# Performance work log

Hardware: AMD Instinct MI355X
Metric: run time of the kernel (lower is better)

## Reference

```python
import jax, jax.numpy as jnp
import numpy as np

NA, NB, D, H = 8192, 2048, 192, 4
DK = D // H


def setup_inputs() -> dict:
    key = jax.random.key(0)
    ks = jax.random.split(key, 12)
    a_z = jax.random.normal(ks[0], (NA, D), dtype=jnp.float32)
    bv_z = jax.random.normal(ks[1], (NB, D), dtype=jnp.float32)
    weight = jax.random.normal(ks[2], (NA, NB), dtype=jnp.float32)
    mask = jax.random.randint(ks[3], (NA, NB), 0, 2).astype(bool)
    mask = mask.at[:, 0].set(True)  # every actor has >=1 valid bill (valid_idx == all)
    s = 1.0 / np.sqrt(D)
    Wq = jax.random.normal(ks[4], (D, D), dtype=jnp.float32) * s
    Wk = jax.random.normal(ks[5], (D, D), dtype=jnp.float32) * s
    Wv = jax.random.normal(ks[6], (D, D), dtype=jnp.float32) * s
    Wo = jax.random.normal(ks[7], (D, D), dtype=jnp.float32) * s
    bq = jnp.zeros((D,), jnp.float32)
    bk = jnp.zeros((D,), jnp.float32)
    bvb = jnp.zeros((D,), jnp.float32)
    bo = jnp.zeros((D,), jnp.float32)
    return {"a_z": a_z, "bv_z": bv_z, "weight": weight, "mask": mask,
            "Wq": Wq, "Wk": Wk, "Wv": Wv, "Wo": Wo,
            "bq": bq, "bk": bk, "bvb": bvb, "bo": bo}


def reference(a_z, bv_z, weight, mask, Wq, Wk, Wv, Wo, bq, bk, bvb, bo):
    # ActorHead.forward: per-actor single-query attention over bill versions,
    # with float attn_mask from `weight` and key_padding_mask from `mask`.
    a_z = jnp.nan_to_num(a_z, nan=0.0, posinf=1.0, neginf=-1.0)
    bv_z = jnp.nan_to_num(bv_z, nan=0.0, posinf=1.0, neginf=-1.0)
    w = jnp.nan_to_num(weight, nan=0.0, posinf=1.0, neginf=-1.0)

    q = (a_z @ Wq.T + bq).reshape(NA, H, DK)   # [NA,H,DK]
    k = (bv_z @ Wk.T + bk).reshape(NB, H, DK)  # [NB,H,DK]
    v = (bv_z @ Wv.T + bvb).reshape(NB, H, DK)

    scores = jnp.einsum('ahd,bhd->ahb', q, k) / np.sqrt(DK)  # [NA,H,NB]
    w_masked = jnp.where(mask, w, -jnp.inf)                  # attn_mask (weight.masked_fill)
    kpm = jnp.where(mask, 0.0, -jnp.inf)                     # key_padding_mask as additive bias
    scores = scores + (w_masked + kpm)[:, None, :]

    p = jax.nn.softmax(scores, axis=-1)                      # [NA,H,NB]
    out = jnp.einsum('ahb,bhd->ahd', p, v).reshape(NA, D)
    out = out @ Wo.T + bo
    out = jnp.nan_to_num(out, nan=0.0, posinf=0.0, neginf=0.0)
    topic_align = out.reshape(NA, H, DK).mean(axis=1)        # [NA,DK]

    attn_avg = jnp.nan_to_num(p.mean(axis=1), nan=0.0, posinf=0.0, neginf=0.0)
    attn_avg = attn_avg * mask
    norm_scores = jax.nn.softmax(w_masked, axis=-1)
    norm_scores = jnp.nan_to_num(norm_scores, nan=0.0, posinf=0.0, neginf=0.0) * mask
    influence = jnp.nan_to_num((norm_scores * attn_avg).sum(axis=-1),
                               nan=0.0, posinf=1.0, neginf=-1.0)  # [NA]

    # pack (topic_align, influence) into one array: [NA, DK+1]
    return jnp.concatenate([topic_align, influence[:, None]], axis=-1)
```

## Files before the change

### kernel.cpp

```cpp
#include <hip/hip_runtime.h>
#include <hip/hip_bf16.h>

#define NA 8192
#define NB 2048
#define DIM 192
#define NH 4
#define DKH 48
#define TA 16
#define TB 32
#define PREC 200
#define SCALE 0.14433756729740643f
#define INVSCALE 6.928203230275509f
#define NEGBIG 1e30f

typedef __bf16 bf16x8 __attribute__((ext_vector_type(8)));
typedef float f32x4 __attribute__((ext_vector_type(4)));

#define MFMA16(a, b, c) __builtin_amdgcn_mfma_f32_16x16x32_bf16(a, b, c, 0, 0, 0)

#define GLDS(gp, lp)                                                      \
  __builtin_amdgcn_global_load_lds(                                       \
      (__attribute__((address_space(1))) void*)(const void*)(gp),         \
      (__attribute__((address_space(3))) void*)(void*)(lp), 16, 0, 0)

__device__ __forceinline__ float rsumg(float v) {
  v += __shfl_xor(v, 16, 64);
  v += __shfl_xor(v, 32, 64);
  return v;
}

__global__ __launch_bounds__(256) void prep_kernel(
    const float* __restrict__ a_z, const float* __restrict__ bv_z,
    const float* __restrict__ Wq, const float* __restrict__ Wk, const float* __restrict__ Wv,
    const float* __restrict__ bq, const float* __restrict__ bk, const float* __restrict__ bvb,
    const float* __restrict__ Wo, const float* __restrict__ bo,
    const float* __restrict__ weight, const void* __restrict__ maskp,
    __bf16* __restrict__ Qo, __bf16* __restrict__ Ko, __bf16* __restrict__ Vo,
    float* __restrict__ WoeT, float* __restrict__ boe, int* __restrict__ mflag,
    float* __restrict__ MwG, float* __restrict__ LwG)
{
  const int blk = blockIdx.x;
  const int t = threadIdx.x;

  if (blk < 1536) {
    __shared__ float xs[8][DIM];
    const float* src; const float* W; const float* bias; int row0; int which;
    if (blk < 1024)      { src = a_z;  W = Wq; bias = bq;  row0 = blk * 8;          which = 0; }
    else if (blk < 1280) { src = bv_z; W = Wk; bias = bk;  row0 = (blk - 1024) * 8; which = 1; }
    else                 { src = bv_z; W = Wv; bias = bvb; row0 = (blk - 1280) * 8; which = 2; }
    for (int i = t; i < 8 * 48; i += 256) {
      int r = i / 48, c = i % 48;
      ((float4*)xs[r])[c] = ((const float4*)(src + (size_t)(row0 + r) * DIM))[c];
    }
    __syncthreads();
    if (t < 192) {
      float acc[8];
      float bb = bias[t];
      #pragma unroll
      for (int r = 0; r < 8; ++r) acc[r] = bb;
      const float4* wr = (const float4*)(W + (size_t)t * DIM);
      for (int c = 0; c < 48; ++c) {
        float4 w = wr[c];
        #pragma unroll
        for (int r = 0; r < 8; ++r) {
          float4 x = ((const float4*)xs[r])[c];
          acc[r] += w.x * x.x + w.y * x.y + w.z * x.z + w.w * x.w;
        }
      }
      int h = t / 48, dd = t % 48;
      if (which == 0) {
        #pragma unroll
        for (int r = 0; r < 8; ++r)
          Qo[((size_t)(row0 + r) * 4 + h) * 64 + dd] = (__bf16)acc[r];
      } else if (which == 1) {
        #pragma unroll
        for (int r = 0; r < 8; ++r)
          Ko[((size_t)h * NB + row0 + r) * 64 + dd] = (__bf16)acc[r];
      } else {
        bf16x8 pk;
        #pragma unroll
        for (int r = 0; r < 8; ++r) pk[r] = (__bf16)acc[r];
        *(bf16x8*)(Vo + (size_t)t * NB + row0) = pk;
      }
    }
    if (which == 0) {
      for (int i = t; i < 512; i += 256) {
        int r = i >> 6, hh = (i >> 4) & 3, kk = i & 15;
        Qo[((size_t)(row0 + r) * 4 + hh) * 64 + 48 + kk] = (__bf16)0.f;
      }
    } else if (which == 1) {
      for (int i = t; i < 512; i += 256) {
        int r = i >> 6, hh = (i >> 4) & 3, kk = i & 15;
        Ko[((size_t)hh * NB + row0 + r) * 64 + 48 + kk] = (__bf16)0.f;
      }
    }
  } else if (blk == 1536) {
    __shared__ int fl;
    if (t == 0) fl = 0;
    __syncthreads();
    const unsigned int* mw = (const unsigned int*)maskp;
    for (int i = t; i < 1024; i += 256) {
      unsigned int v = mw[i];
      if (v == 0x3F800000u) atomicMax(&fl, 2);
      else if (v > 1u) atomicMax(&fl, 1);
    }
    __syncthreads();
    if (t == 0) *mflag = fl;
  } else if (blk < 1573) {
    int i = (blk - 1537) * 256 + t;
    if (i < DIM * DKH) {
      int k = i / DKH, d = i % DKH;
      float s = 0.25f * (Wo[(size_t)d * DIM + k] + Wo[(size_t)(d + 48) * DIM + k] +
                         Wo[(size_t)(d + 96) * DIM + k] + Wo[(size_t)(d + 144) * DIM + k]);
      WoeT[k * DKH + d] = s;
    }
    if (i < DKH) boe[i] = 0.25f * (bo[i] + bo[i + 48] + bo[i + 96] + bo[i + 144]);
  } else {
    __shared__ int fl;
    if (t == 0) fl = 0;
    __syncthreads();
    {
      const unsigned int* mw = (const unsigned int*)maskp;
      for (int i = t; i < 1024; i += 256) {
        unsigned int v = mw[i];
        if (v == 0x3F800000u) atomicMax(&fl, 2);
        else if (v > 1u) atomicMax(&fl, 1);
      }
    }
    __syncthreads();
    const int mmode = fl;
    const int lane = t & 63;
    const int a = (blk - 1573) * 4 + (t >> 6);
    const float* wr = weight + (size_t)a * NB;
    const unsigned char* m8 = (const unsigned char*)maskp + (size_t)a * NB;
    const float* mf = (const float*)maskp + (size_t)a * NB;
    const int* m32 = (const int*)maskp + (size_t)a * NB;

    float mloc = -NEGBIG, sloc = 0.f;
    for (int it = 0; it < 8; ++it) {
      int idx = it * 256 + lane * 4;
      float4 w4 = *(const float4*)(wr + idx);
      bool ok0, ok1, ok2, ok3;
      if (mmode == 1) {
        unsigned mm = *(const unsigned*)(m8 + idx);
        ok0 = mm & 0xffu; ok1 = (mm >> 8) & 0xffu; ok2 = (mm >> 16) & 0xffu; ok3 = mm >> 24;
      } else if (mmode == 2) {
        float4 mv = *(const float4*)(mf + idx);
        ok0 = mv.x != 0.f; ok1 = mv.y != 0.f; ok2 = mv.z != 0.f; ok3 = mv.w != 0.f;
      } else {
        int4 mv = *(const int4*)(m32 + idx);
        ok0 = mv.x; ok1 = mv.y; ok2 = mv.z; ok3 = mv.w;
      }
      float v0 = ok0 ? w4.x : -NEGBIG;
      float v1 = ok1 ? w4.y : -NEGBIG;
      float v2 = ok2 ? w4.z : -NEGBIG;
      float v3 = ok3 ? w4.w : -NEGBIG;
      float mt = fmaxf(fmaxf(v0, v1), fmaxf(v2, v3));
      float mn = fmaxf(mloc, mt);
      float sc = __expf(mloc - mn);
      float e0 = (v0 > -1e29f) ? __expf(v0 - mn) : 0.f;
      float e1 = (v1 > -1e29f) ? __expf(v1 - mn) : 0.f;
      float e2 = (v2 > -1e29f) ? __expf(v2 - mn) : 0.f;
      float e3 = (v3 > -1e29f) ? __expf(v3 - mn) : 0.f;
      sloc = sloc * sc + (e0 + e1) + (e2 + e3);
      mloc = mn;
    }
    float mfin = mloc;
    #pragma unroll
    for (int off = 1; off < 64; off <<= 1) mfin = fmaxf(mfin, __shfl_xor(mfin, off, 64));
    float sadj = sloc * __expf(mloc - mfin);
    #pragma unroll
    for (int off = 1; off < 64; off <<= 1) sadj += __shfl_xor(sadj, off, 64);
    if (lane == 0) { MwG[a] = mfin; LwG[a] = sadj; }
  }
}

__global__ __launch_bounds__(256) void vw_kernel(
    const __bf16* __restrict__ Vt, const float* __restrict__ WoeT, __bf16* __restrict__ VWt)
{
  __shared__ float woe[DIM][DKH];
  const int t = threadIdx.x;
  for (int i = t; i < DIM * DKH / 4; i += 256)
    ((float4*)&woe[0][0])[i] = ((const float4*)WoeT)[i];
  __syncthreads();
  const int b = blockIdx.x * 16 + (t & 15);
  const int grp = t >> 4;
  const int h = grp >> 2;
  const int q = grp & 3;
  float acc[12];
  #pragma unroll
  for (int d = 0; d < 12; ++d) acc[d] = 0.f;
  for (int dp = 0; dp < DKH; ++dp) {
    float v = (float)Vt[(size_t)(h * DKH + dp) * NB + b];
    const float* wrow = &woe[h * DKH + dp][q * 12];
    #pragma unroll
    for (int d = 0; d < 12; ++d) acc[d] += v * wrow[d];
  }
  #pragma unroll
  for (int d = 0; d < 12; ++d)
    VWt[(size_t)(h * DKH + q * 12 + d) * NB + b] = (__bf16)acc[d];
}

template<int MMODE>
__global__ __launch_bounds__(256, 4) void attn_kernel(
    const __bf16* __restrict__ Qb, const __bf16* __restrict__ Kb, const __bf16* __restrict__ VWt,
    const float* __restrict__ weight, const void* __restrict__ maskp,
    const int* __restrict__ maskflag, const float* __restrict__ MwG,
    float* __restrict__ part, int tps)
{
  if (*maskflag != MMODE) return;

  __shared__ __align__(16) __bf16 Kl[4 * 32 * 64];
  __shared__ __align__(16) __bf16 VWl[192 * 32];
  __shared__ __bf16 Ss[4][16][40];

  const int t = threadIdx.x;
  const int lane = t & 63;
  const int h = t >> 6;
  const int c = lane & 15;
  const int g = lane >> 4;
  const int g8 = g * 8;
  const int s = blockIdx.x >> 9;
  const int a0 = (blockIdx.x & 511) * TA;
  const int tile0 = s * tps;
  const int tend = tile0 + tps;

  const unsigned char* m8 = (const unsigned char*)maskp;
  const float* mfp = (const float*)maskp;
  const int* m32 = (const int*)maskp;

  const __bf16* qp = Qb + ((size_t)(a0 + c) * NH + h) * 64 + g8;
  const bf16x8 qf0 = *(const bf16x8*)qp;
  const bf16x8 qf1 = *(const bf16x8*)(qp + 32);

  const float MwC = MwG[a0 + c];
  float lp = 0.f, Ap = 0.f;
  f32x4 o0 = {0.f,0.f,0.f,0.f}, o1 = {0.f,0.f,0.f,0.f}, o2 = {0.f,0.f,0.f,0.f};

  const size_t wrow = (size_t)(a0 + c) * NB + g * 4;

  const int kswz = 8 * ((lane & 7) ^ ((lane >> 3) & 7));
  const int vswz = 8 * ((lane & 3) ^ ((lane >> 3) & 3));
  const size_t kgrow = (size_t)h * NB + (lane >> 3);
  const size_t vgrow = (size_t)(h * 48 + (lane >> 2)) * NB;
  __bf16* klw = Kl + h * 2048;
  __bf16* vlw = VWl + h * 1536;

  const int swk  = 8 * (g ^ (c & 7));
  const int swk4 = 8 * ((g | 4) ^ (c & 7));
  const int swv  = 8 * (g ^ ((c >> 1) & 3));
  const __bf16* klr = Kl + h * 2048 + c * 64;
  const __bf16* vlr = VWl + (h * 48 + c) * 32 + swv;

  float4 nw0, nw1;
  int nmx, nmy;
  int4 nmA, nmB;
  {
    size_t gi = wrow + (size_t)tile0 * TB;
    nw0 = *(const float4*)(weight + gi);
    nw1 = *(const float4*)(weight + gi + 16);
    if constexpr (MMODE == 1)      { nmx = *(const int*)(m8 + gi); nmy = *(const int*)(m8 + gi + 16); }
    else if constexpr (MMODE == 2) { nmA = *(const int4*)(mfp + gi); nmB = *(const int4*)(mfp + gi + 16); }
    else                           { nmA = *(const int4*)(m32 + gi); nmB = *(const int4*)(m32 + gi + 16); }
  }

  for (int tile = tile0; tile < tend; ++tile) {
    const int b0 = tile * TB;

    {
      const __bf16* kg = Kb + (kgrow + b0) * 64 + kswz;
      GLDS(kg,            klw);
      GLDS(kg + 8 * 64,   klw + 512);
      GLDS(kg + 16 * 64,  klw + 1024);
      GLDS(kg + 24 * 64,  klw + 1536);
      const __bf16* vg = VWt + vgrow + b0 + vswz;
      GLDS(vg,            vlw);
      GLDS(vg + 16 * NB,  vlw + 512);
      GLDS(vg + 32 * NB,  vlw + 1024);
    }
    __builtin_amdgcn_sched_barrier(0);

    float wv[8];
    if constexpr (MMODE == 1) {
      unsigned ua = (unsigned)nmx, ub = (unsigned)nmy;
      wv[0] = (ua & 0xffu)         ? nw0.x : -NEGBIG;
      wv[1] = ((ua >> 8) & 0xffu)  ? nw0.y : -NEGBIG;
      wv[2] = ((ua >> 16) & 0xffu) ? nw0.z : -NEGBIG;
      wv[3] = (ua >> 24)           ? nw0.w : -NEGBIG;
      wv[4] = (ub & 0xffu)         ? nw1.x : -NEGBIG;
      wv[5] = ((ub >> 8) & 0xffu)  ? nw1.y : -NEGBIG;
      wv[6] = ((ub >> 16) & 0xffu) ? nw1.z : -NEGBIG;
      wv[7] = (ub >> 24)           ? nw1.w : -NEGBIG;
    } else if constexpr (MMODE == 2) {
      wv[0] = (((unsigned)nmA.x << 1) != 0u) ? nw0.x : -NEGBIG;
      wv[1] = (((unsigned)nmA.y << 1) != 0u) ? nw0.y : -NEGBIG;
      wv[2] = (((unsigned)nmA.z << 1) != 0u) ? nw0.z : -NEGBIG;
      wv[3] = (((unsigned)nmA.w << 1) != 0u) ? nw0.w : -NEGBIG;
      wv[4] = (((unsigned)nmB.x << 1) != 0u) ? nw1.x : -NEGBIG;
      wv[5] = (((unsigned)nmB.y << 1) != 0u) ? nw1.y : -NEGBIG;
      wv[6] = (((unsigned)nmB.z << 1) != 0u) ? nw1.z : -NEGBIG;
      wv[7] = (((unsigned)nmB.w << 1) != 0u) ? nw1.w : -NEGBIG;
    } else {
      wv[0] = nmA.x ? nw0.x : -NEGBIG;
      wv[1] = nmA.y ? nw0.y : -NEGBIG;
      wv[2] = nmA.z ? nw0.z : -NEGBIG;
      wv[3] = nmA.w ? nw0.w : -NEGBIG;
      wv[4] = nmB.x ? nw1.x : -NEGBIG;
      wv[5] = nmB.y ? nw1.y : -NEGBIG;
      wv[6] = nmB.z ? nw1.z : -NEGBIG;
      wv[7] = nmB.w ? nw1.w : -NEGBIG;
    }
    __builtin_amdgcn_sched_barrier(0);

    {
      int tn = (tile + 1 < tend) ? tile + 1 : tile;
      size_t gi = wrow + (size_t)tn * TB;
      nw0 = *(const float4*)(weight + gi);
      nw1 = *(const float4*)(weight + gi + 16);
      if constexpr (MMODE == 1)      { nmx = *(const int*)(m8 + gi); nmy = *(const int*)(m8 + gi + 16); }
      else if constexpr (MMODE == 2) { nmA = *(const int4*)(mfp + gi); nmB = *(const int4*)(mfp + gi + 16); }
      else                           { nmA = *(const int4*)(m32 + gi); nmB = *(const int4*)(m32 + gi + 16); }
    }
    __builtin_amdgcn_sched_barrier(0);

    asm volatile("s_waitcnt vmcnt(4)" ::: "memory");
    __builtin_amdgcn_sched_barrier(0);

    bf16x8 kA0 = *(const bf16x8*)(klr + swk);
    bf16x8 kA1 = *(const bf16x8*)(klr + swk4);
    bf16x8 kB0 = *(const bf16x8*)(klr + 16 * 64 + swk);
    bf16x8 kB1 = *(const bf16x8*)(klr + 16 * 64 + swk4);
    bf16x8 vf0 = *(const bf16x8*)vlr;
    bf16x8 vf1 = *(const bf16x8*)(vlr + 16 * 32);
    bf16x8 vf2 = *(const bf16x8*)(vlr + 32 * 32);

    f32x4 acc0, acc1;
    #pragma unroll
    for (int j = 0; j < 4; ++j) { acc0[j] = wv[j] * INVSCALE; acc1[j] = wv[4 + j] * INVSCALE; }
    acc0 = MFMA16(kA0, qf0, acc0);
    acc0 = MFMA16(kA1, qf1, acc0);
    acc1 = MFMA16(kB0, qf0, acc1);
    acc1 = MFMA16(kB1, qf1, acc1);

    float p[8];
    #pragma unroll
    for (int j = 0; j < 4; ++j) {
      float s0 = acc0[j] * SCALE, s1 = acc1[j] * SCALE;
      float p0 = __expf(s0), p1 = __expf(s1);
      lp += p0 + p1;
      Ap += __expf(s0 + wv[j] - MwC) + __expf(s1 + wv[4 + j] - MwC);
      p[j] = p0; p[4 + j] = p1;
    }

    #pragma unroll
    for (int i = 0; i < 4; ++i) {
      Ss[h][c][g * 4 + i]      = (__bf16)p[i];
      Ss[h][c][16 + g * 4 + i] = (__bf16)p[4 + i];
    }
    __builtin_amdgcn_sched_barrier(0);
    bf16x8 pb = *(const bf16x8*)&Ss[h][c][g8];

    o0 = MFMA16(vf0, pb, o0);
    o1 = MFMA16(vf1, pb, o1);
    o2 = MFMA16(vf2, pb, o2);
  }

  float l = rsumg(lp);
  float A = rsumg(Ap);
  float* pr = part + ((size_t)s * NA + a0 + c) * PREC;
  #pragma unroll
  for (int j = 0; j < 4; ++j) {
    pr[h * 48 + g * 4 + j]      = o0[j];
    pr[h * 48 + 16 + g * 4 + j] = o1[j];
    pr[h * 48 + 32 + g * 4 + j] = o2[j];
  }
  if (g == 0) {
    pr[192 + h] = l;
    pr[196 + h] = A;
  }
}

__global__ __launch_bounds__(256) void merge_kernel(
    const float* __restrict__ part, const float* __restrict__ LwG,
    const float* __restrict__ boe, float* __restrict__ out, int ns)
{
  __shared__ float fls[32][NH];
  __shared__ float infl[32][NH];
  const int t = threadIdx.x;
  const int a0 = blockIdx.x * 32;

  if (t < 128) {
    int a = t >> 2, hh = t & 3;
    const float* rec = part + (size_t)(a0 + a) * PREC;
    float lst = 0.f, As = 0.f;
    for (int s = 0; s < ns; ++s) {
      const float* r = rec + (size_t)s * NA * PREC;
      lst += r[192 + hh];
      As  += r[196 + hh];
    }
    float li = 1.f / lst;
    fls[a][hh] = li;
    infl[a][hh] = As * li;
  }
  __syncthreads();
  if (t < 32)
    out[(size_t)(a0 + t) * 49 + 48] =
        (infl[t][0] + infl[t][1] + infl[t][2] + infl[t][3]) / (4.f * LwG[a0 + t]);
  for (int i = t; i < 32 * DKH; i += 256) {
    int a = i / DKH, dd = i - a * DKH;
    float acc = boe[dd];
    const float* rec = part + (size_t)(a0 + a) * PREC;
    for (int s = 0; s < ns; ++s) {
      const float* r = rec + (size_t)s * NA * PREC;
      #pragma unroll
      for (int hh = 0; hh < NH; ++hh)
        acc += fls[a][hh] * r[hh * 48 + dd];
    }
    out[(size_t)(a0 + a) * 49 + dd] = acc;
  }
}

extern "C" void kernel_launch(void* const* d_in, const int* in_sizes, int n_in,
                              void* d_out, int out_size, void* d_ws, size_t ws_size,
                              hipStream_t stream) {
  const float* a_z    = (const float*)d_in[0];
  const float* bv_z   = (const float*)d_in[1];
  const float* weight = (const float*)d_in[2];
  const void*  maskp  = d_in[3];
  const float* Wq = (const float*)d_in[4];
  const float* Wk = (const float*)d_in[5];
  const float* Wv = (const float*)d_in[6];
  const float* Wo = (const float*)d_in[7];
  const float* bq = (const float*)d_in[8];
  const float* bk = (const float*)d_in[9];
  const float* bvb = (const float*)d_in[10];
  const float* bo = (const float*)d_in[11];

  __bf16* Qb  = (__bf16*)d_ws;
  __bf16* Kb  = Qb + (size_t)NA * 256;
  __bf16* Vtg = Kb + (size_t)4 * NB * 64;
  __bf16* VWt = Vtg + (size_t)DIM * NB;
  float* WoeT = (float*)(VWt + (size_t)DIM * NB);
  float* boe  = WoeT + DIM * DKH;
  int*  mflag = (int*)(boe + 64);
  float* MwG  = (float*)(mflag + 64);
  float* LwG  = MwG + NA;
  float* part = LwG + NA;

  size_t base = (size_t)((char*)(part) - (char*)d_ws);
  int ns = (ws_size >= base + (size_t)4 * NA * PREC * 4) ? 4 : 2;
  int tps = (NB / TB) / ns;

  prep_kernel<<<3621, 256, 0, stream>>>(a_z, bv_z, Wq, Wk, Wv, bq, bk, bvb, Wo, bo,
                                        weight, maskp, Qb, Kb, Vtg, WoeT, boe, mflag,
                                        MwG, LwG);
  vw_kernel<<<NB / 16, 256, 0, stream>>>(Vtg, WoeT, VWt);
  attn_kernel<1><<<ns * 512, 256, 0, stream>>>(Qb, Kb, VWt, weight, maskp, mflag, MwG, part, tps);
  attn_kernel<0><<<ns * 512, 256, 0, stream>>>(Qb, Kb, VWt, weight, maskp, mflag, MwG, part, tps);
  attn_kernel<2><<<ns * 512, 256, 0, stream>>>(Qb, Kb, VWt, weight, maskp, mflag, MwG, part, tps);
  merge_kernel<<<NA / 32, 256, 0, stream>>>(part, LwG, boe, (float*)d_out, ns);
}
```

Measured before the change: 175.9 us.

## Fold weight-softmax normalizer into attention pass, drop separate max/sum pre-pass

Removes the prep-kernel blocks that streamed the full weight and mask matrices to compute a per-row max and sum for the weight softmax. Instead the attention kernel computes exp(w) once per element, multiplies it into the score exponential and accumulates the weight-softmax denominator as an extra partial, which the merge kernel then sums. This avoids a second full read of the 64 MB weight matrix plus its mask. The trade-off is that exp(w) and exp(score) are taken without subtracting a running max, so large weight or score values could overflow where the previous max-shifted form would not.

After: 165.6 us (median of 2 runs). 1.06x faster.

```diff
diff --git a/kernel.cpp b/kernel.cpp
--- a/kernel.cpp
+++ b/kernel.cpp
@@ -8,9 +8,8 @@
 #define DKH 48
 #define TA 16
 #define TB 32
-#define PREC 200
+#define PREC 204
 #define SCALE 0.14433756729740643f
-#define INVSCALE 6.928203230275509f
 #define NEGBIG 1e30f
 
 typedef __bf16 bf16x8 __attribute__((ext_vector_type(8)));
@@ -34,10 +33,9 @@
     const float* __restrict__ Wq, const float* __restrict__ Wk, const float* __restrict__ Wv,
     const float* __restrict__ bq, const float* __restrict__ bk, const float* __restrict__ bvb,
     const float* __restrict__ Wo, const float* __restrict__ bo,
-    const float* __restrict__ weight, const void* __restrict__ maskp,
+    const void* __restrict__ maskp,
     __bf16* __restrict__ Qo, __bf16* __restrict__ Ko, __bf16* __restrict__ Vo,
-    float* __restrict__ WoeT, float* __restrict__ boe, int* __restrict__ mflag,
-    float* __restrict__ MwG, float* __restrict__ LwG)
+    float* __restrict__ WoeT, float* __restrict__ boe, int* __restrict__ mflag)
 {
   const int blk = blockIdx.x;
   const int t = threadIdx.x;
@@ -106,7 +104,7 @@
     }
     __syncthreads();
     if (t == 0) *mflag = fl;
-  } else if (blk < 1573) {
+  } else {
     int i = (blk - 1537) * 256 + t;
     if (i < DIM * DKH) {
       int k = i / DKH, d = i % DKH;
@@ -115,63 +113,6 @@
       WoeT[k * DKH + d] = s;
     }
     if (i < DKH) boe[i] = 0.25f * (bo[i] + bo[i + 48] + bo[i + 96] + bo[i + 144]);
-  } else {
-    __shared__ int fl;
-    if (t == 0) fl = 0;
-    __syncthreads();
-    {
-      const unsigned int* mw = (const unsigned int*)maskp;
-      for (int i = t; i < 1024; i += 256) {
-        unsigned int v = mw[i];
-        if (v == 0x3F800000u) atomicMax(&fl, 2);
-        else if (v > 1u) atomicMax(&fl, 1);
-      }
-    }
-    __syncthreads();
-    const int mmode = fl;
-    const int lane = t & 63;
-    const int a = (blk - 1573) * 4 + (t >> 6);
-    const float* wr = weight + (size_t)a * NB;
-    const unsigned char* m8 = (const unsigned char*)maskp + (size_t)a * NB;
-    const float* mf = (const float*)maskp + (size_t)a * NB;
-    const int* m32 = (const int*)maskp + (size_t)a * NB;
-
-    float mloc = -NEGBIG, sloc = 0.f;
-    for (int it = 0; it < 8; ++it) {
-      int idx = it * 256 + lane * 4;
-      float4 w4 = *(const float4*)(wr + idx);
-      bool ok0, ok1, ok2, ok3;
-      if (mmode == 1) {
-        unsigned mm = *(const unsigned*)(m8 + idx);
-        ok0 = mm & 0xffu; ok1 = (mm >> 8) & 0xffu; ok2 = (mm >> 16) & 0xffu; ok3 = mm >> 24;
-      } else if (mmode == 2) {
-        float4 mv = *(const float4*)(mf + idx);
-        ok0 = mv.x != 0.f; ok1 = mv.y != 0.f; ok2 = mv.z != 0.f; ok3 = mv.w != 0.f;
-      } else {
-        int4 mv = *(const int4*)(m32 + idx);
-        ok0 = mv.x; ok1 = mv.y; ok2 = mv.z; ok3 = mv.w;
-      }
-      float v0 = ok0 ? w4.x : -NEGBIG;
-      float v1 = ok1 ? w4.y : -NEGBIG;
-      float v2 = ok2 ? w4.z : -NEGBIG;
-      float v3 = ok3 ? w4.w : -NEGBIG;
-      float mt = fmaxf(fmaxf(v0, v1), fmaxf(v2, v3));
-      float mn = fmaxf(mloc, mt);
-      float sc = __expf(mloc - mn);
-      float e0 = (v0 > -1e29f) ? __expf(v0 - mn) : 0.f;
-      float e1 = (v1 > -1e29f) ? __expf(v1 - mn) : 0.f;
-      float e2 = (v2 > -1e29f) ? __expf(v2 - mn) : 0.f;
-      float e3 = (v3 > -1e29f) ? __expf(v3 - mn) : 0.f;
-      sloc = sloc * sc + (e0 + e1) + (e2 + e3);
-      mloc = mn;
-    }
-    float mfin = mloc;
-    #pragma unroll
-    for (int off = 1; off < 64; off <<= 1) mfin = fmaxf(mfin, __shfl_xor(mfin, off, 64));
-    float sadj = sloc * __expf(mloc - mfin);
-    #pragma unroll
-    for (int off = 1; off < 64; off <<= 1) sadj += __shfl_xor(sadj, off, 64);
-    if (lane == 0) { MwG[a] = mfin; LwG[a] = sadj; }
   }
 }
 
@@ -205,7 +146,7 @@
 __global__ __launch_bounds__(256, 4) void attn_kernel(
     const __bf16* __restrict__ Qb, const __bf16* __restrict__ Kb, const __bf16* __restrict__ VWt,
     const float* __restrict__ weight, const void* __restrict__ maskp,
-    const int* __restrict__ maskflag, const float* __restrict__ MwG,
+    const int* __restrict__ maskflag,
     float* __restrict__ part, int tps)
 {
   if (*maskflag != MMODE) return;
@@ -233,8 +174,7 @@
   const bf16x8 qf0 = *(const bf16x8*)qp;
   const bf16x8 qf1 = *(const bf16x8*)(qp + 32);
 
-  const float MwC = MwG[a0 + c];
-  float lp = 0.f, Ap = 0.f;
+  float lp = 0.f, Ap = 0.f, Lwp = 0.f;
   f32x4 o0 = {0.f,0.f,0.f,0.f}, o1 = {0.f,0.f,0.f,0.f}, o2 = {0.f,0.f,0.f,0.f};
 
   const size_t wrow = (size_t)(a0 + c) * NB + g * 4;
@@ -280,35 +220,35 @@
     }
     __builtin_amdgcn_sched_barrier(0);
 
-    float wv[8];
+    float ew[8];
     if constexpr (MMODE == 1) {
       unsigned ua = (unsigned)nmx, ub = (unsigned)nmy;
-      wv[0] = (ua & 0xffu)         ? nw0.x : -NEGBIG;
-      wv[1] = ((ua >> 8) & 0xffu)  ? nw0.y : -NEGBIG;
-      wv[2] = ((ua >> 16) & 0xffu) ? nw0.z : -NEGBIG;
-      wv[3] = (ua >> 24)           ? nw0.w : -NEGBIG;
-      wv[4] = (ub & 0xffu)         ? nw1.x : -NEGBIG;
-      wv[5] = ((ub >> 8) & 0xffu)  ? nw1.y : -NEGBIG;
-      wv[6] = ((ub >> 16) & 0xffu) ? nw1.z : -NEGBIG;
-      wv[7] = (ub >> 24)           ? nw1.w : -NEGBIG;
+      ew[0] = (ua & 0xffu)         ? __expf(nw0.x) : 0.f;
+      ew[1] = ((ua >> 8) & 0xffu)  ? __expf(nw0.y) : 0.f;
+      ew[2] = ((ua >> 16) & 0xffu) ? __expf(nw0.z) : 0.f;
+      ew[3] = (ua >> 24)           ? __expf(nw0.w) : 0.f;
+      ew[4] = (ub & 0xffu)         ? __expf(nw1.x) : 0.f;
+      ew[5] = ((ub >> 8) & 0xffu)  ? __expf(nw1.y) : 0.f;
+      ew[6] = ((ub >> 16) & 0xffu) ? __expf(nw1.z) : 0.f;
+      ew[7] = (ub >> 24)           ? __expf(nw1.w) : 0.f;
     } else if constexpr (MMODE == 2) {
-      wv[0] = (((unsigned)nmA.x << 1) != 0u) ? nw0.x : -NEGBIG;
-      wv[1] = (((unsigned)nmA.y << 1) != 0u) ? nw0.y : -NEGBIG;
-      wv[2] = (((unsigned)nmA.z << 1) != 0u) ? nw0.z : -NEGBIG;
-      wv[3] = (((unsigned)nmA.w << 1) != 0u) ? nw0.w : -NEGBIG;
-      wv[4] = (((unsigned)nmB.x << 1) != 0u) ? nw1.x : -NEGBIG;
-      wv[5] = (((unsigned)nmB.y << 1) != 0u) ? nw1.y : -NEGBIG;
-      wv[6] = (((unsigned)nmB.z << 1) != 0u) ? nw1.z : -NEGBIG;
-      wv[7] = (((unsigned)nmB.w << 1) != 0u) ? nw1.w : -NEGBIG;
+      ew[0] = (((unsigned)nmA.x << 1) != 0u) ? __expf(nw0.x) : 0.f;
+      ew[1] = (((unsigned)nmA.y << 1) != 0u) ? __expf(nw0.y) : 0.f;
+      ew[2] = (((unsigned)nmA.z << 1) != 0u) ? __expf(nw0.z) : 0.f;
+      ew[3] = (((unsigned)nmA.w << 1) != 0u) ? __expf(nw0.w) : 0.f;
+      ew[4] = (((unsigned)nmB.x << 1) != 0u) ? __expf(nw1.x) : 0.f;
+      ew[5] = (((unsigned)nmB.y << 1) != 0u) ? __expf(nw1.y) : 0.f;
+      ew[6] = (((unsigned)nmB.z << 1) != 0u) ? __expf(nw1.z) : 0.f;
+      ew[7] = (((unsigned)nmB.w << 1) != 0u) ? __expf(nw1.w) : 0.f;
     } else {
-      wv[0] = nmA.x ? nw0.x : -NEGBIG;
-      wv[1] = nmA.y ? nw0.y : -NEGBIG;
-      wv[2] = nmA.z ? nw0.z : -NEGBIG;
-      wv[3] = nmA.w ? nw0.w : -NEGBIG;
-      wv[4] = nmB.x ? nw1.x : -NEGBIG;
-      wv[5] = nmB.y ? nw1.y : -NEGBIG;
-      wv[6] = nmB.z ? nw1.z : -NEGBIG;
-      wv[7] = nmB.w ? nw1.w : -NEGBIG;
+      ew[0] = nmA.x ? __expf(nw0.x) : 0.f;
+      ew[1] = nmA.y ? __expf(nw0.y) : 0.f;
+      ew[2] = nmA.z ? __expf(nw0.z) : 0.f;
+      ew[3] = nmA.w ? __expf(nw0.w) : 0.f;
+      ew[4] = nmB.x ? __expf(nw1.x) : 0.f;
+      ew[5] = nmB.y ? __expf(nw1.y) : 0.f;
+      ew[6] = nmB.z ? __expf(nw1.z) : 0.f;
+      ew[7] = nmB.w ? __expf(nw1.w) : 0.f;
     }
     __builtin_amdgcn_sched_barrier(0);
 
@@ -334,28 +274,30 @@
     bf16x8 vf1 = *(const bf16x8*)(vlr + 16 * 32);
     bf16x8 vf2 = *(const bf16x8*)(vlr + 32 * 32);
 
-    f32x4 acc0, acc1;
-    #pragma unroll
-    for (int j = 0; j < 4; ++j) { acc0[j] = wv[j] * INVSCALE; acc1[j] = wv[4 + j] * INVSCALE; }
+    f32x4 acc0 = {0.f,0.f,0.f,0.f}, acc1 = {0.f,0.f,0.f,0.f};
     acc0 = MFMA16(kA0, qf0, acc0);
     acc0 = MFMA16(kA1, qf1, acc0);
     acc1 = MFMA16(kB0, qf0, acc1);
     acc1 = MFMA16(kB1, qf1, acc1);
 
-    float p[8];
+    Lwp += (ew[0] + ew[1]) + (ew[2] + ew[3]) + (ew[4] + ew[5]) + (ew[6] + ew[7]);
+
+    float pt[8];
     #pragma unroll
     for (int j = 0; j < 4; ++j) {
-      float s0 = acc0[j] * SCALE, s1 = acc1[j] * SCALE;
-      float p0 = __expf(s0), p1 = __expf(s1);
+      float e0 = __expf(acc0[j] * SCALE);
+      float e1 = __expf(acc1[j] * SCALE);
+      float p0 = e0 * ew[j];
+      float p1 = e1 * ew[4 + j];
       lp += p0 + p1;
-      Ap += __expf(s0 + wv[j] - MwC) + __expf(s1 + wv[4 + j] - MwC);
-      p[j] = p0; p[4 + j] = p1;
+      Ap += p0 * ew[j] + p1 * ew[4 + j];
+      pt[j] = p0; pt[4 + j] = p1;
     }
 
     #pragma unroll
     for (int i = 0; i < 4; ++i) {
-      Ss[h][c][g * 4 + i]      = (__bf16)p[i];
-      Ss[h][c][16 + g * 4 + i] = (__bf16)p[4 + i];
+      Ss[h][c][g * 4 + i]      = (__bf16)pt[i];
+      Ss[h][c][16 + g * 4 + i] = (__bf16)pt[4 + i];
     }
     __builtin_amdgcn_sched_barrier(0);
     bf16x8 pb = *(const bf16x8*)&Ss[h][c][g8];
@@ -367,6 +309,7 @@
 
   float l = rsumg(lp);
   float A = rsumg(Ap);
+  float Lw = rsumg(Lwp);
   float* pr = part + ((size_t)s * NA + a0 + c) * PREC;
   #pragma unroll
   for (int j = 0; j < 4; ++j) {
@@ -377,35 +320,39 @@
   if (g == 0) {
     pr[192 + h] = l;
     pr[196 + h] = A;
+    if (h == 0) pr[200] = Lw;
   }
 }
 
 __global__ __launch_bounds__(256) void merge_kernel(
-    const float* __restrict__ part, const float* __restrict__ LwG,
-    const float* __restrict__ boe, float* __restrict__ out, int ns)
+    const float* __restrict__ part, const float* __restrict__ boe,
+    float* __restrict__ out, int ns)
 {
   __shared__ float fls[32][NH];
   __shared__ float infl[32][NH];
+  __shared__ float lws[32];
   const int t = threadIdx.x;
   const int a0 = blockIdx.x * 32;
 
   if (t < 128) {
     int a = t >> 2, hh = t & 3;
     const float* rec = part + (size_t)(a0 + a) * PREC;
-    float lst = 0.f, As = 0.f;
+    float lst = 0.f, As = 0.f, Lws = 0.f;
     for (int s = 0; s < ns; ++s) {
       const float* r = rec + (size_t)s * NA * PREC;
       lst += r[192 + hh];
       As  += r[196 + hh];
+      if (hh == 0) Lws += r[200];
     }
     float li = 1.f / lst;
     fls[a][hh] = li;
     infl[a][hh] = As * li;
+    if (hh == 0) lws[a] = Lws;
   }
   __syncthreads();
   if (t < 32)
     out[(size_t)(a0 + t) * 49 + 48] =
-        (infl[t][0] + infl[t][1] + infl[t][2] + infl[t][3]) / (4.f * LwG[a0 + t]);
+        (infl[t][0] + infl[t][1] + infl[t][2] + infl[t][3]) / (4.f * lws[t]);
   for (int i = t; i < 32 * DKH; i += 256) {
     int a = i / DKH, dd = i - a * DKH;
     float acc = boe[dd];
@@ -443,20 +390,17 @@
   float* WoeT = (float*)(VWt + (size_t)DIM * NB);
   float* boe  = WoeT + DIM * DKH;
   int*  mflag = (int*)(boe + 64);
-  float* MwG  = (float*)(mflag + 64);
-  float* LwG  = MwG + NA;
-  float* part = LwG + NA;
+  float* part = (float*)(mflag + 64);
 
   size_t base = (size_t)((char*)(part) - (char*)d_ws);
   int ns = (ws_size >= base + (size_t)4 * NA * PREC * 4) ? 4 : 2;
   int tps = (NB / TB) / ns;
 
-  prep_kernel<<<3621, 256, 0, stream>>>(a_z, bv_z, Wq, Wk, Wv, bq, bk, bvb, Wo, bo,
-                                        weight, maskp, Qb, Kb, Vtg, WoeT, boe, mflag,
-                                        MwG, LwG);
+  prep_kernel<<<1573, 256, 0, stream>>>(a_z, bv_z, Wq, Wk, Wv, bq, bk, bvb, Wo, bo,
+                                        maskp, Qb, Kb, Vtg, WoeT, boe, mflag);
   vw_kernel<<<NB / 16, 256, 0, stream>>>(Vtg, WoeT, VWt);
-  attn_kernel<1><<<ns * 512, 256, 0, stream>>>(Qb, Kb, VWt, weight, maskp, mflag, MwG, part, tps);
-  attn_kernel<0><<<ns * 512, 256, 0, stream>>>(Qb, Kb, VWt, weight, maskp, mflag, MwG, part, tps);
-  attn_kernel<2><<<ns * 512, 256, 0, stream>>>(Qb, Kb, VWt, weight, maskp, mflag, MwG, part, tps);
-  merge_kernel<<<NA / 32, 256, 0, stream>>>(part, LwG, boe, (float*)d_out, ns);
-}
+  attn_kernel<1><<<ns * 512, 256, 0, stream>>>(Qb, Kb, VWt, weight, maskp, mflag, part, tps);
+  attn_kernel<0><<<ns * 512, 256, 0, stream>>>(Qb, Kb, VWt, weight, maskp, mflag, part, tps);
+  attn_kernel<2><<<ns * 512, 256, 0, stream>>>(Qb, Kb, VWt, weight, maskp, mflag, part, tps);
+  merge_kernel<<<NA / 32, 256, 0, stream>>>(part, boe, (float*)d_out, ns);
+}
```
